# Kernel optimization log

Measured on AMD Instinct MI355X. Metric: run time of the kernel, lower is better.

Reference implementation:

```python
import jax, jax.numpy as jnp
import numpy as np

SUPPORT_NUM = 4
EPS = 1e-12


def _normalize(x, axis):
    n = jnp.linalg.norm(x, axis=axis, keepdims=True)
    return x / jnp.maximum(n, EPS)


def _gather_neighbors(tensor, index):
    # tensor: (bs, v, d), index: (bs, v, n) -> (bs, v, n, d)
    return jax.vmap(lambda t, i: t[i])(tensor, index)


def setup_inputs() -> dict:
    key = jax.random.key(0)
    ks = jax.random.split(key, 12)
    bs, v, n = 4, 4096, 50
    in_c, out_c, sup = 64, 64, SUPPORT_NUM
    stdv = 1.0 / np.sqrt(out_c * (sup + 1))
    u = lambda k, shape, s: jax.random.uniform(k, shape, jnp.float32, -s, s)
    return {
        "neighbor_index": jax.random.randint(ks[0], (bs, v, n), 0, v),
        "vertices": jax.random.normal(ks[1], (bs, v, 3), jnp.float32),
        "feature_map": jax.random.normal(ks[2], (bs, v, in_c), jnp.float32),
        "neighbor_value": jax.random.normal(ks[3], (bs, v, n), jnp.float32),
        "weights": u(ks[4], (in_c, (sup + 1) * out_c), stdv),
        "bias": u(ks[5], ((sup + 1) * out_c,), stdv),
        "directions": u(ks[6], (3, sup * out_c), stdv),
        "l1_w": u(ks[7], (n, n), 1.0 / np.sqrt(n)),
        "l1_b": u(ks[8], (n,), 1.0 / np.sqrt(n)),
        "l2_w": u(ks[9], (n, n), 1.0 / np.sqrt(n)),
        "l2_b": u(ks[10], (n,), 1.0 / np.sqrt(n)),
    }


def reference(neighbor_index, vertices, feature_map, neighbor_value,
              weights, bias, directions, l1_w, l1_b, l2_w, l2_b):
    bs, v, n = neighbor_index.shape
    out_c = bias.shape[0] // (SUPPORT_NUM + 1)

    # neighbor direction (unit vectors): (bs, v, n, 3)
    neighbors = _gather_neighbors(vertices, neighbor_index)
    ndn = _normalize(neighbors - vertices[:, :, None, :], axis=-1)

    # theta: (bs, v, n, support*out)
    sdn = _normalize(directions, axis=0)
    theta = jax.nn.relu(ndn @ sdn)

    feature_out = feature_map @ weights + bias  # (bs, v, (S+1)*out)
    feature_center = feature_out[:, :, :out_c]
    feature_support = _gather_neighbors(feature_out[:, :, out_c:], neighbor_index)

    neighbor_value = _normalize(neighbor_value, axis=-1)
    # original computes the MLP but discards it (weight is reassigned); kept for fidelity
    _unused = jax.nn.relu(jax.nn.relu(neighbor_value @ l1_w.T + l1_b) @ l2_w.T + l2_b)
    weight = _normalize(neighbor_value, axis=-1)  # (bs, v, n)

    act = theta * feature_support * weight[..., None]  # (bs, v, n, S*out)
    act = act.reshape(bs, v, n, SUPPORT_NUM, out_c).sum(axis=(2, 3))  # (bs, v, out)
    return feature_center + act
```

## Files before the change

### kernel.cpp

```cpp
#include <hip/hip_runtime.h>
#include <math.h>

#define BS   4
#define V    4096
#define NB   50
#define IC   64
#define OC   64
#define SUP  4
#define WCOL 320
#define WT_STRIDE 72

typedef float    f32x4 __attribute__((ext_vector_type(4)));
typedef short    s16x8 __attribute__((ext_vector_type(8)));
typedef _Float16 h16x2 __attribute__((ext_vector_type(2)));

__device__ inline unsigned short bf16r(float f) {
    unsigned u = __builtin_bit_cast(unsigned, f);
    u += 0x7FFFu + ((u >> 16) & 1u);
    return (unsigned short)(u >> 16);
}
__device__ inline unsigned short f16b(float f) {
    return __builtin_bit_cast(unsigned short, (_Float16)f);
}
__device__ inline float fdot2acc(h16x2 a, h16x2 b, float c) {
#if __has_builtin(__builtin_amdgcn_fdot2)
    return __builtin_amdgcn_fdot2(a, b, c, false);
#else
    return c + (float)a.x * (float)b.x + (float)a.y * (float)b.y;
#endif
}

__global__ __launch_bounds__(256) void feat_kernel(
    const float* __restrict__ fm,
    const float* __restrict__ W,
    const float* __restrict__ bias,
    float* __restrict__ out,
    unsigned short* __restrict__ fo_s)
{
    __shared__ unsigned short wt[WCOL * WT_STRIDE];
    const int t = threadIdx.x;

#pragma unroll
    for (int i = 0; i < 20; ++i) {
        const int idx4 = t + i * 256;
        const int e    = idx4 * 4;
        const int k    = e / WCOL;
        const int col  = e - k * WCOL;
        const float4 v = reinterpret_cast<const float4*>(W)[idx4];
        wt[(col + 0) * WT_STRIDE + k] = bf16r(v.x);
        wt[(col + 1) * WT_STRIDE + k] = bf16r(v.y);
        wt[(col + 2) * WT_STRIDE + k] = bf16r(v.z);
        wt[(col + 3) * WT_STRIDE + k] = bf16r(v.w);
    }
    __syncthreads();

    const int w   = t >> 6;
    const int l   = t & 63;
    const int rlo = l & 15;
    const int kg  = l >> 4;
    const int row = blockIdx.x * 64 + w * 16 + rlo;

    const float* fr = &fm[row * IC + kg * 8];
    s16x8 a0, a1;
#pragma unroll
    for (int e = 0; e < 8; ++e) {
        a0[e] = (short)bf16r(fr[e]);
        a1[e] = (short)bf16r(fr[32 + e]);
    }

    const int drow0 = blockIdx.x * 64 + w * 16 + kg * 4;
#pragma unroll
    for (int ct = 0; ct < 20; ++ct) {
        const int col = ct * 16 + rlo;
        const s16x8 b0 = *reinterpret_cast<const s16x8*>(&wt[col * WT_STRIDE + kg * 8]);
        const s16x8 b1 = *reinterpret_cast<const s16x8*>(&wt[col * WT_STRIDE + 32 + kg * 8]);
        f32x4 acc = {0.f, 0.f, 0.f, 0.f};
        acc = __builtin_amdgcn_mfma_f32_16x16x32_bf16(a0, b0, acc, 0, 0, 0);
        acc = __builtin_amdgcn_mfma_f32_16x16x32_bf16(a1, b1, acc, 0, 0, 0);
        const float bv = bias[col];
        if (ct < 4) {
#pragma unroll
            for (int r = 0; r < 4; ++r)
                out[(drow0 + r) * OC + col] = acc[r] + bv;
        } else {
            const int cc = (col - OC) & 63;
            const int s  = (col - OC) >> 6;
#pragma unroll
            for (int r = 0; r < 4; ++r)
                fo_s[((drow0 + r) * OC + cc) * SUP + s] =
                    __builtin_bit_cast(unsigned short, (_Float16)(acc[r] + bv));
        }
    }
}

__global__ __launch_bounds__(256) void conv_kernel(
    const int*   __restrict__ nidx,
    const float* __restrict__ verts,
    const float* __restrict__ nval,
    const float* __restrict__ dirs,
    const unsigned short* __restrict__ fo_s,
    float* __restrict__ out)
{
    const int bid  = blockIdx.x;
    const int swz  = ((bid & 7) << 8) + (bid >> 3);
    const int wv   = threadIdx.x >> 6;
    const int l    = threadIdx.x & 63;
    const int row0 = swz * 8 + wv * 2;
    const int row1 = row0 + 1;
    const int b    = row0 >> 12;

    h16x2 cs01x, cs01y, cs01z, cs23x, cs23y, cs23z;
    {
        float sx[4], sy[4], sz[4];
#pragma unroll
        for (int s = 0; s < 4; ++s) {
            const int col = s * 64 + l;
            const float d0 = dirs[col], d1 = dirs[256 + col], d2 = dirs[512 + col];
            const float inv = 1.f / fmaxf(sqrtf(d0 * d0 + d1 * d1 + d2 * d2), 1e-12f);
            sx[s] = d0 * inv; sy[s] = d1 * inv; sz[s] = d2 * inv;
        }
        cs01x = (h16x2){ (_Float16)sx[0], (_Float16)sx[1] };
        cs01y = (h16x2){ (_Float16)sy[0], (_Float16)sy[1] };
        cs01z = (h16x2){ (_Float16)sz[0], (_Float16)sz[1] };
        cs23x = (h16x2){ (_Float16)sx[2], (_Float16)sx[3] };
        cs23y = (h16x2){ (_Float16)sy[2], (_Float16)sy[3] };
        cs23z = (h16x2){ (_Float16)sz[2], (_Float16)sz[3] };
    }

    unsigned ex0, ey0, ez0, eo0, ex1, ey1, ez1, eo1;
    {
        auto setup = [&](int row, unsigned& ux, unsigned& uy,
                         unsigned& uz, unsigned& uo) {
            const float nv = (l < NB) ? nval[(size_t)row * NB + l] : 0.f;
            float ss = nv * nv;
#pragma unroll
            for (int o = 32; o > 0; o >>= 1) ss += __shfl_xor(ss, o);
            const float wn = nv * (1.f / fmaxf(sqrtf(ss), 1e-12f));
            ux = uy = uz = uo = 0u;
            if (l < NB) {
                const int idx = nidx[(size_t)row * NB + l];
                const float* vn = &verts[(size_t)(b * V + idx) * 3];
                const float* vc = &verts[(size_t)row * 3];
                float dx = vn[0] - vc[0], dy = vn[1] - vc[1], dz = vn[2] - vc[2];
                const float inv = 1.f / fmaxf(sqrtf(dx*dx + dy*dy + dz*dz), 1e-12f);
                dx *= inv; dy *= inv; dz *= inv;
                const unsigned hx = f16b(dx), hy = f16b(dy);
                const unsigned hzv = f16b(dz), hw = f16b(wn);
                ux = hx | (hx << 16);
                uy = hy | (hy << 16);
                uz = hzv | (hw << 16);
                uo = ((unsigned)idx) << 9;
            }
        };
        setup(row0, ex0, ey0, ez0, eo0);
        setup(row1, ex1, ey1, ez1, eo1);
    }

    const float ctr0 = out[(size_t)row0 * OC + l];
    const float ctr1 = out[(size_t)row1 * OC + l];

    const char* baseb = (const char*)fo_s + (size_t)b * ((size_t)V * OC * SUP * 2);
    const unsigned c8 = (unsigned)(l << 3);

    float a00 = 0.f, a01 = 0.f, a10 = 0.f, a11 = 0.f;
    const h16x2 hz = { (_Float16)0.f, (_Float16)0.f };

#define ROWOP(EX, EY, EZ, EO, A0, A1) { \
        const unsigned ax = (unsigned)__builtin_amdgcn_readlane((int)(EX), j); \
        const unsigned ay = (unsigned)__builtin_amdgcn_readlane((int)(EY), j); \
        const unsigned az = (unsigned)__builtin_amdgcn_readlane((int)(EZ), j); \
        const unsigned ao = (unsigned)__builtin_amdgcn_readlane((int)(EO), j); \
        const h16x2 dxdx = __builtin_bit_cast(h16x2, ax); \
        const h16x2 dydy = __builtin_bit_cast(h16x2, ay); \
        const unsigned zlo = az & 0xffffu, zhi = az >> 16; \
        const h16x2 dzdz = __builtin_bit_cast(h16x2, zlo | (zlo << 16)); \
        const h16x2 wjwj = __builtin_bit_cast(h16x2, zhi | (zhi << 16)); \
        h16x2 t01 = dxdx * cs01x + dydy * cs01y + dzdz * cs01z; \
        h16x2 t23 = dxdx * cs23x + dydy * cs23y + dzdz * cs23z; \
        t01 = __builtin_elementwise_max(t01, hz); \
        t23 = __builtin_elementwise_max(t23, hz); \
        t01 *= wjwj; t23 *= wjwj; \
        const uint2 gg = *reinterpret_cast<const uint2*>(baseb + (size_t)(ao + c8)); \
        A0 = fdot2acc(t01, __builtin_bit_cast(h16x2, gg.x), A0); \
        A1 = fdot2acc(t23, __builtin_bit_cast(h16x2, gg.y), A1); }

#pragma unroll
    for (int j = 0; j < NB; ++j) {
        ROWOP(ex0, ey0, ez0, eo0, a00, a01)
        ROWOP(ex1, ey1, ez1, eo1, a10, a11)
    }
#undef ROWOP

    out[(size_t)row0 * OC + l] = ctr0 + a00 + a01;
    out[(size_t)row1 * OC + l] = ctr1 + a10 + a11;
}

extern "C" void kernel_launch(void* const* d_in, const int* in_sizes, int n_in,
                              void* d_out, int out_size, void* d_ws, size_t ws_size,
                              hipStream_t stream) {
    const int*   nidx  = (const int*)  d_in[0];
    const float* verts = (const float*)d_in[1];
    const float* fm    = (const float*)d_in[2];
    const float* nval  = (const float*)d_in[3];
    const float* W     = (const float*)d_in[4];
    const float* bias  = (const float*)d_in[5];
    const float* dirs  = (const float*)d_in[6];
    float*       out   = (float*)d_out;

    unsigned short* fo_s = (unsigned short*)d_ws;

    feat_kernel<<<(BS * V) / 64, 256, 0, stream>>>(fm, W, bias, out, fo_s);
    conv_kernel<<<(BS * V) / 8, 256, 0, stream>>>(nidx, verts, nval, dirs,
                                                  fo_s, out);
}
```

Measured before the change: 52.25 us.

## Double-buffer neighbor feature gathers into LDS via async global_load_lds

The conv kernel now gives each wave one output row instead of two. Neighbor feature rows are fetched with direct global-to-LDS loads in chunks of 10 neighbors, double-buffered, with explicit vmcnt waits so the next chunk's gathers overlap compute on the current one. The goal is to hide gather latency better than the previous per-neighbor register loads did. In exchange it uses more blocks, adds LDS traffic and hand-placed waitcnt/sched barriers, and gives up the two-row interleaving that previously supplied ILP.

New measurement: 59.28 us. 1.13x slower.

```diff
diff --git a/kernel.cpp b/kernel.cpp
--- a/kernel.cpp
+++ b/kernel.cpp
@@ -9,10 +9,14 @@
 #define SUP  4
 #define WCOL 320
 #define WT_STRIDE 72
+#define CH   10
 
 typedef float    f32x4 __attribute__((ext_vector_type(4)));
 typedef short    s16x8 __attribute__((ext_vector_type(8)));
 typedef _Float16 h16x2 __attribute__((ext_vector_type(2)));
+
+typedef const __attribute__((address_space(1))) unsigned GU;
+typedef __attribute__((address_space(3))) unsigned LU;
 
 __device__ inline unsigned short bf16r(float f) {
     unsigned u = __builtin_bit_cast(unsigned, f);
@@ -28,6 +32,9 @@
 #else
     return c + (float)a.x * (float)b.x + (float)a.y * (float)b.y;
 #endif
+}
+__device__ inline void gll4(const void* g, void* l) {
+    __builtin_amdgcn_global_load_lds((GU*)g, (LU*)l, 4, 0, 0);
 }
 
 __global__ __launch_bounds__(256) void feat_kernel(
@@ -101,13 +108,16 @@
     const unsigned short* __restrict__ fo_s,
     float* __restrict__ out)
 {
-    const int bid  = blockIdx.x;
-    const int swz  = ((bid & 7) << 8) + (bid >> 3);
-    const int wv   = threadIdx.x >> 6;
-    const int l    = threadIdx.x & 63;
-    const int row0 = swz * 8 + wv * 2;
-    const int row1 = row0 + 1;
-    const int b    = row0 >> 12;
+    const int bid = blockIdx.x;
+    const int swz = ((bid & 7) << 9) + (bid >> 3);
+    const int wv  = threadIdx.x >> 6;
+    const int l   = threadIdx.x & 63;
+    const int row = swz * 4 + wv;
+    const int b   = swz >> 10;
+
+    __shared__ uint4 sbuf[4][2][CH * 32];
+    char* const b0p = (char*)&sbuf[wv][0][0];
+    char* const b1p = (char*)&sbuf[wv][1][0];
 
     h16x2 cs01x, cs01y, cs01z, cs23x, cs23y, cs23z;
     {
@@ -127,49 +137,51 @@
         cs23z = (h16x2){ (_Float16)sz[2], (_Float16)sz[3] };
     }
 
-    unsigned ex0, ey0, ez0, eo0, ex1, ey1, ez1, eo1;
+    unsigned ex = 0, ey = 0, ez = 0, eo = 0;
     {
-        auto setup = [&](int row, unsigned& ux, unsigned& uy,
-                         unsigned& uz, unsigned& uo) {
-            const float nv = (l < NB) ? nval[(size_t)row * NB + l] : 0.f;
-            float ss = nv * nv;
-#pragma unroll
-            for (int o = 32; o > 0; o >>= 1) ss += __shfl_xor(ss, o);
-            const float wn = nv * (1.f / fmaxf(sqrtf(ss), 1e-12f));
-            ux = uy = uz = uo = 0u;
-            if (l < NB) {
-                const int idx = nidx[(size_t)row * NB + l];
-                const float* vn = &verts[(size_t)(b * V + idx) * 3];
-                const float* vc = &verts[(size_t)row * 3];
-                float dx = vn[0] - vc[0], dy = vn[1] - vc[1], dz = vn[2] - vc[2];
-                const float inv = 1.f / fmaxf(sqrtf(dx*dx + dy*dy + dz*dz), 1e-12f);
-                dx *= inv; dy *= inv; dz *= inv;
-                const unsigned hx = f16b(dx), hy = f16b(dy);
-                const unsigned hzv = f16b(dz), hw = f16b(wn);
-                ux = hx | (hx << 16);
-                uy = hy | (hy << 16);
-                uz = hzv | (hw << 16);
-                uo = ((unsigned)idx) << 9;
-            }
-        };
-        setup(row0, ex0, ey0, ez0, eo0);
-        setup(row1, ex1, ey1, ez1, eo1);
-    }
-
-    const float ctr0 = out[(size_t)row0 * OC + l];
-    const float ctr1 = out[(size_t)row1 * OC + l];
-
-    const char* baseb = (const char*)fo_s + (size_t)b * ((size_t)V * OC * SUP * 2);
-    const unsigned c8 = (unsigned)(l << 3);
-
-    float a00 = 0.f, a01 = 0.f, a10 = 0.f, a11 = 0.f;
+        const float nv = (l < NB) ? nval[(size_t)row * NB + l] : 0.f;
+        float ss = nv * nv;
+#pragma unroll
+        for (int o = 32; o > 0; o >>= 1) ss += __shfl_xor(ss, o);
+        const float wn = nv * (1.f / fmaxf(sqrtf(ss), 1e-12f));
+        if (l < NB) {
+            const int idx = nidx[(size_t)row * NB + l];
+            const float* vn = &verts[(size_t)(b * V + idx) * 3];
+            const float* vc = &verts[(size_t)row * 3];
+            float dx = vn[0] - vc[0], dy = vn[1] - vc[1], dz = vn[2] - vc[2];
+            const float inv = 1.f / fmaxf(sqrtf(dx*dx + dy*dy + dz*dz), 1e-12f);
+            dx *= inv; dy *= inv; dz *= inv;
+            const unsigned hx = f16b(dx), hy = f16b(dy);
+            const unsigned hzv = f16b(dz), hw = f16b(wn);
+            ex = hx | (hx << 16);
+            ey = hy | (hy << 16);
+            ez = hzv | (hw << 16);
+            eo = ((unsigned)idx) << 9;
+        }
+    }
+
+    const float ctr = out[(size_t)row * OC + l];
+
+    const char* gbase = (const char*)fo_s + (size_t)b * ((size_t)V * OC * SUP * 2);
+    const unsigned l4 = (unsigned)(l << 2);
+
+    float acc0 = 0.f, acc1 = 0.f;
     const h16x2 hz = { (_Float16)0.f, (_Float16)0.f };
 
-#define ROWOP(EX, EY, EZ, EO, A0, A1) { \
-        const unsigned ax = (unsigned)__builtin_amdgcn_readlane((int)(EX), j); \
-        const unsigned ay = (unsigned)__builtin_amdgcn_readlane((int)(EY), j); \
-        const unsigned az = (unsigned)__builtin_amdgcn_readlane((int)(EZ), j); \
-        const unsigned ao = (unsigned)__builtin_amdgcn_readlane((int)(EO), j); \
+#define ISSUE(T, BUFP) _Pragma("unroll") \
+    for (int jj = 0; jj < CH; ++jj) { \
+        const unsigned off = (unsigned)__builtin_amdgcn_readlane((int)eo, (T) * CH + jj); \
+        const char* g = gbase + (size_t)(off + l4); \
+        gll4(g,       BUFP + jj * 512); \
+        gll4(g + 256, BUFP + jj * 512 + 256); \
+    }
+
+#define CCHUNK(T, BUFP) _Pragma("unroll") \
+    for (int jj = 0; jj < CH; ++jj) { \
+        const int j = (T) * CH + jj; \
+        const unsigned ax = (unsigned)__builtin_amdgcn_readlane((int)ex, j); \
+        const unsigned ay = (unsigned)__builtin_amdgcn_readlane((int)ey, j); \
+        const unsigned az = (unsigned)__builtin_amdgcn_readlane((int)ez, j); \
         const h16x2 dxdx = __builtin_bit_cast(h16x2, ax); \
         const h16x2 dydy = __builtin_bit_cast(h16x2, ay); \
         const unsigned zlo = az & 0xffffu, zhi = az >> 16; \
@@ -180,19 +192,32 @@
         t01 = __builtin_elementwise_max(t01, hz); \
         t23 = __builtin_elementwise_max(t23, hz); \
         t01 *= wjwj; t23 *= wjwj; \
-        const uint2 gg = *reinterpret_cast<const uint2*>(baseb + (size_t)(ao + c8)); \
-        A0 = fdot2acc(t01, __builtin_bit_cast(h16x2, gg.x), A0); \
-        A1 = fdot2acc(t23, __builtin_bit_cast(h16x2, gg.y), A1); }
-
-#pragma unroll
-    for (int j = 0; j < NB; ++j) {
-        ROWOP(ex0, ey0, ez0, eo0, a00, a01)
-        ROWOP(ex1, ey1, ez1, eo1, a10, a11)
-    }
-#undef ROWOP
-
-    out[(size_t)row0 * OC + l] = ctr0 + a00 + a01;
-    out[(size_t)row1 * OC + l] = ctr1 + a10 + a11;
+        const uint2 gg = *reinterpret_cast<const uint2*>(BUFP + jj * 512 + (l << 3)); \
+        acc0 = fdot2acc(t01, __builtin_bit_cast(h16x2, gg.x), acc0); \
+        acc1 = fdot2acc(t23, __builtin_bit_cast(h16x2, gg.y), acc1); \
+    }
+
+#define WAIT20 { asm volatile("s_waitcnt vmcnt(20)" ::: "memory"); \
+                 __builtin_amdgcn_sched_barrier(0); }
+#define WAIT0  { asm volatile("s_waitcnt vmcnt(0)"  ::: "memory"); \
+                 __builtin_amdgcn_sched_barrier(0); }
+#define LDRAIN { asm volatile("s_waitcnt lgkmcnt(0)" ::: "memory"); \
+                 __builtin_amdgcn_sched_barrier(0); }
+
+    ISSUE(0, b0p)
+    ISSUE(1, b1p) WAIT20 CCHUNK(0, b0p) LDRAIN
+    ISSUE(2, b0p) WAIT20 CCHUNK(1, b1p) LDRAIN
+    ISSUE(3, b1p) WAIT20 CCHUNK(2, b0p) LDRAIN
+    ISSUE(4, b0p) WAIT20 CCHUNK(3, b1p) LDRAIN
+                  WAIT0  CCHUNK(4, b0p)
+
+#undef ISSUE
+#undef CCHUNK
+#undef WAIT20
+#undef WAIT0
+#undef LDRAIN
+
+    out[(size_t)row * OC + l] = ctr + acc0 + acc1;
 }
 
 extern "C" void kernel_launch(void* const* d_in, const int* in_sizes, int n_in,
@@ -210,6 +235,6 @@
     unsigned short* fo_s = (unsigned short*)d_ws;
 
     feat_kernel<<<(BS * V) / 64, 256, 0, stream>>>(fm, W, bias, out, fo_s);
-    conv_kernel<<<(BS * V) / 8, 256, 0, stream>>>(nidx, verts, nval, dirs,
+    conv_kernel<<<(BS * V) / 4, 256, 0, stream>>>(nidx, verts, nval, dirs,
                                                   fo_s, out);
 }
```

## Split wave into row halves with 16-byte gathers and LDS-staged neighbor data

Applied to the files above, without the earlier changes.

The conv kernel now gives each half-wave one row. Each lane handles two output channels and reads a 16-byte uint4 gather per neighbor instead of an 8-byte one. Per-neighbor direction, weight and offset values are staged in shared memory and read back as broadcasts, replacing the readlane SGPR broadcasts. The goal is to halve the number of gather instructions and cut scalar/readlane overhead per neighbor. In exchange it adds LDS traffic, doubles the direction registers per lane, and relies on the LDS writes being visible within the wave without a barrier.

New measurement: 48.70 us. -6.8%, faster.

```diff
diff --git a/kernel.cpp b/kernel.cpp
--- a/kernel.cpp
+++ b/kernel.cpp
@@ -21,6 +21,9 @@
 }
 __device__ inline unsigned short f16b(float f) {
     return __builtin_bit_cast(unsigned short, (_Float16)f);
+}
+__device__ inline h16x2 bch(unsigned u) {
+    return __builtin_bit_cast(h16x2, u);
 }
 __device__ inline float fdot2acc(h16x2 a, h16x2 b, float c) {
 #if __has_builtin(__builtin_amdgcn_fdot2)
@@ -105,94 +108,108 @@
     const int swz  = ((bid & 7) << 8) + (bid >> 3);
     const int wv   = threadIdx.x >> 6;
     const int l    = threadIdx.x & 63;
+    const int half = l >> 5;
+    const int m    = l & 31;
+    const int c0   = m * 2;
     const int row0 = swz * 8 + wv * 2;
-    const int row1 = row0 + 1;
+    const int row  = row0 + half;
     const int b    = row0 >> 12;
 
-    h16x2 cs01x, cs01y, cs01z, cs23x, cs23y, cs23z;
+    __shared__ uint4    tb [4][2][NB];
+    __shared__ unsigned tbo[4][2][NB];
+
+    h16x2 ax01, ay01, az01, ax23, ay23, az23;
+    h16x2 bx01, by01, bz01, bx23, by23, bz23;
     {
-        float sx[4], sy[4], sz[4];
+        float sx0[4], sy0[4], sz0[4], sx1[4], sy1[4], sz1[4];
 #pragma unroll
         for (int s = 0; s < 4; ++s) {
-            const int col = s * 64 + l;
-            const float d0 = dirs[col], d1 = dirs[256 + col], d2 = dirs[512 + col];
-            const float inv = 1.f / fmaxf(sqrtf(d0 * d0 + d1 * d1 + d2 * d2), 1e-12f);
-            sx[s] = d0 * inv; sy[s] = d1 * inv; sz[s] = d2 * inv;
+            const int col = s * 64 + c0;
+            const float2 d0 = *reinterpret_cast<const float2*>(&dirs[col]);
+            const float2 d1 = *reinterpret_cast<const float2*>(&dirs[256 + col]);
+            const float2 d2 = *reinterpret_cast<const float2*>(&dirs[512 + col]);
+            const float i0 = 1.f / fmaxf(sqrtf(d0.x*d0.x + d1.x*d1.x + d2.x*d2.x), 1e-12f);
+            const float i1 = 1.f / fmaxf(sqrtf(d0.y*d0.y + d1.y*d1.y + d2.y*d2.y), 1e-12f);
+            sx0[s] = d0.x * i0; sy0[s] = d1.x * i0; sz0[s] = d2.x * i0;
+            sx1[s] = d0.y * i1; sy1[s] = d1.y * i1; sz1[s] = d2.y * i1;
         }
-        cs01x = (h16x2){ (_Float16)sx[0], (_Float16)sx[1] };
-        cs01y = (h16x2){ (_Float16)sy[0], (_Float16)sy[1] };
-        cs01z = (h16x2){ (_Float16)sz[0], (_Float16)sz[1] };
-        cs23x = (h16x2){ (_Float16)sx[2], (_Float16)sx[3] };
-        cs23y = (h16x2){ (_Float16)sy[2], (_Float16)sy[3] };
-        cs23z = (h16x2){ (_Float16)sz[2], (_Float16)sz[3] };
-    }
-
-    unsigned ex0, ey0, ez0, eo0, ex1, ey1, ez1, eo1;
-    {
-        auto setup = [&](int row, unsigned& ux, unsigned& uy,
-                         unsigned& uz, unsigned& uo) {
-            const float nv = (l < NB) ? nval[(size_t)row * NB + l] : 0.f;
-            float ss = nv * nv;
-#pragma unroll
-            for (int o = 32; o > 0; o >>= 1) ss += __shfl_xor(ss, o);
-            const float wn = nv * (1.f / fmaxf(sqrtf(ss), 1e-12f));
-            ux = uy = uz = uo = 0u;
-            if (l < NB) {
-                const int idx = nidx[(size_t)row * NB + l];
-                const float* vn = &verts[(size_t)(b * V + idx) * 3];
-                const float* vc = &verts[(size_t)row * 3];
-                float dx = vn[0] - vc[0], dy = vn[1] - vc[1], dz = vn[2] - vc[2];
-                const float inv = 1.f / fmaxf(sqrtf(dx*dx + dy*dy + dz*dz), 1e-12f);
-                dx *= inv; dy *= inv; dz *= inv;
-                const unsigned hx = f16b(dx), hy = f16b(dy);
-                const unsigned hzv = f16b(dz), hw = f16b(wn);
-                ux = hx | (hx << 16);
-                uy = hy | (hy << 16);
-                uz = hzv | (hw << 16);
-                uo = ((unsigned)idx) << 9;
-            }
-        };
-        setup(row0, ex0, ey0, ez0, eo0);
-        setup(row1, ex1, ey1, ez1, eo1);
-    }
-
-    const float ctr0 = out[(size_t)row0 * OC + l];
-    const float ctr1 = out[(size_t)row1 * OC + l];
-
-    const char* baseb = (const char*)fo_s + (size_t)b * ((size_t)V * OC * SUP * 2);
-    const unsigned c8 = (unsigned)(l << 3);
-
-    float a00 = 0.f, a01 = 0.f, a10 = 0.f, a11 = 0.f;
+        ax01 = (h16x2){(_Float16)sx0[0], (_Float16)sx0[1]};
+        ax23 = (h16x2){(_Float16)sx0[2], (_Float16)sx0[3]};
+        ay01 = (h16x2){(_Float16)sy0[0], (_Float16)sy0[1]};
+        ay23 = (h16x2){(_Float16)sy0[2], (_Float16)sy0[3]};
+        az01 = (h16x2){(_Float16)sz0[0], (_Float16)sz0[1]};
+        az23 = (h16x2){(_Float16)sz0[2], (_Float16)sz0[3]};
+        bx01 = (h16x2){(_Float16)sx1[0], (_Float16)sx1[1]};
+        bx23 = (h16x2){(_Float16)sx1[2], (_Float16)sx1[3]};
+        by01 = (h16x2){(_Float16)sy1[0], (_Float16)sy1[1]};
+        by23 = (h16x2){(_Float16)sy1[2], (_Float16)sy1[3]};
+        bz01 = (h16x2){(_Float16)sz1[0], (_Float16)sz1[1]};
+        bz23 = (h16x2){(_Float16)sz1[2], (_Float16)sz1[3]};
+    }
+
+#pragma unroll
+    for (int ri = 0; ri < 2; ++ri) {
+        const int r = row0 + ri;
+        const float nv = (l < NB) ? nval[(size_t)r * NB + l] : 0.f;
+        float ss = nv * nv;
+#pragma unroll
+        for (int o = 32; o > 0; o >>= 1) ss += __shfl_xor(ss, o);
+        const float wn = nv * (1.f / fmaxf(sqrtf(ss), 1e-12f));
+        if (l < NB) {
+            const int idx = nidx[(size_t)r * NB + l];
+            const float* vn = &verts[(size_t)(b * V + idx) * 3];
+            const float* vc = &verts[(size_t)r * 3];
+            float dx = vn[0] - vc[0], dy = vn[1] - vc[1], dz = vn[2] - vc[2];
+            const float inv = 1.f / fmaxf(sqrtf(dx*dx + dy*dy + dz*dz), 1e-12f);
+            dx *= inv; dy *= inv; dz *= inv;
+            const unsigned hx = f16b(dx), hy = f16b(dy);
+            const unsigned hzv = f16b(dz), hw = f16b(wn);
+            uint4 e;
+            e.x = hx  | (hx  << 16);
+            e.y = hy  | (hy  << 16);
+            e.z = hzv | (hzv << 16);
+            e.w = hw  | (hw  << 16);
+            tb [wv][ri][l] = e;
+            tbo[wv][ri][l] = ((unsigned)idx) << 9;
+        }
+    }
+
+    const float2 ctr = *reinterpret_cast<const float2*>(&out[(size_t)row * OC + c0]);
+
+    const char* gb = (const char*)fo_s + (size_t)b * ((size_t)V * OC * SUP * 2)
+                   + (unsigned)(m << 4);
+
+    float acc0 = 0.f, acc1 = 0.f;
     const h16x2 hz = { (_Float16)0.f, (_Float16)0.f };
 
-#define ROWOP(EX, EY, EZ, EO, A0, A1) { \
-        const unsigned ax = (unsigned)__builtin_amdgcn_readlane((int)(EX), j); \
-        const unsigned ay = (unsigned)__builtin_amdgcn_readlane((int)(EY), j); \
-        const unsigned az = (unsigned)__builtin_amdgcn_readlane((int)(EZ), j); \
-        const unsigned ao = (unsigned)__builtin_amdgcn_readlane((int)(EO), j); \
-        const h16x2 dxdx = __builtin_bit_cast(h16x2, ax); \
-        const h16x2 dydy = __builtin_bit_cast(h16x2, ay); \
-        const unsigned zlo = az & 0xffffu, zhi = az >> 16; \
-        const h16x2 dzdz = __builtin_bit_cast(h16x2, zlo | (zlo << 16)); \
-        const h16x2 wjwj = __builtin_bit_cast(h16x2, zhi | (zhi << 16)); \
-        h16x2 t01 = dxdx * cs01x + dydy * cs01y + dzdz * cs01z; \
-        h16x2 t23 = dxdx * cs23x + dydy * cs23y + dzdz * cs23z; \
-        t01 = __builtin_elementwise_max(t01, hz); \
-        t23 = __builtin_elementwise_max(t23, hz); \
-        t01 *= wjwj; t23 *= wjwj; \
-        const uint2 gg = *reinterpret_cast<const uint2*>(baseb + (size_t)(ao + c8)); \
-        A0 = fdot2acc(t01, __builtin_bit_cast(h16x2, gg.x), A0); \
-        A1 = fdot2acc(t23, __builtin_bit_cast(h16x2, gg.y), A1); }
-
 #pragma unroll
     for (int j = 0; j < NB; ++j) {
-        ROWOP(ex0, ey0, ez0, eo0, a00, a01)
-        ROWOP(ex1, ey1, ez1, eo1, a10, a11)
-    }
-#undef ROWOP
-
-    out[(size_t)row0 * OC + l] = ctr0 + a00 + a01;
-    out[(size_t)row1 * OC + l] = ctr1 + a10 + a11;
+        const uint4    e   = tb [wv][half][j];
+        const unsigned off = tbo[wv][half][j];
+        const h16x2 dxdx = bch(e.x), dydy = bch(e.y);
+        const h16x2 dzdz = bch(e.z), wjwj = bch(e.w);
+
+        const uint4 g = *reinterpret_cast<const uint4*>(gb + off);
+
+        h16x2 t01a = dxdx * ax01 + dydy * ay01 + dzdz * az01;
+        h16x2 t23a = dxdx * ax23 + dydy * ay23 + dzdz * az23;
+        h16x2 t01b = dxdx * bx01 + dydy * by01 + dzdz * bz01;
+        h16x2 t23b = dxdx * bx23 + dydy * by23 + dzdz * bz23;
+        t01a = __builtin_elementwise_max(t01a, hz) * wjwj;
+        t23a = __builtin_elementwise_max(t23a, hz) * wjwj;
+        t01b = __builtin_elementwise_max(t01b, hz) * wjwj;
+        t23b = __builtin_elementwise_max(t23b, hz) * wjwj;
+
+        acc0 = fdot2acc(t01a, bch(g.x), acc0);
+        acc0 = fdot2acc(t23a, bch(g.y), acc0);
+        acc1 = fdot2acc(t01b, bch(g.z), acc1);
+        acc1 = fdot2acc(t23b, bch(g.w), acc1);
+    }
+
+    float2 res;
+    res.x = ctr.x + acc0;
+    res.y = ctr.y + acc1;
+    *reinterpret_cast<float2*>(&out[(size_t)row * OC + c0]) = res;
 }
 
 extern "C" void kernel_launch(void* const* d_in, const int* in_sizes, int n_in,
```
